# Kernel optimization log

Measured on AMD Instinct MI355X. Metric: run time of the kernel, lower is better.

Reference implementation:

```python
import jax, jax.numpy as jnp
import numpy as np

N = 6144   # number of patches (bag size)
L = 1024   # input feature dim
D = 512    # GCN hidden dim
ALPHA = 0.4
THRESH = 0.5


def _layernorm(x, g, b):
    m = jnp.mean(x, axis=-1, keepdims=True)
    v = jnp.mean((x - m) ** 2, axis=-1, keepdims=True)
    return (x - m) / jnp.sqrt(v + 1e-5) * g + b


def _l1rows(x):
    # F.normalize(x, p=1): row-wise L1 normalize with eps=1e-12
    return x / jnp.maximum(jnp.sum(jnp.abs(x), axis=1, keepdims=True), 1e-12)


def _nonlin(x, w1, b1, g, bn, w2, b2):
    h = jax.nn.relu(_layernorm(x @ w1 + b1, g, bn))
    return h @ w2 + b2


def _gcn(x, adj, w, b, g, bn):
    # GraphConvolution: adj @ (x @ W) + bias, then LayerNorm + ReLU
    return jax.nn.relu(_layernorm(adj @ (x @ w) + b, g, bn))


def setup_inputs() -> dict:
    key = jax.random.key(0)
    ks = iter(jax.random.split(key, 64))

    def nrm(shape, s=0.02):
        return jax.random.normal(next(ks), shape, jnp.float32) * s

    inp = {
        'x_path': jax.random.normal(next(ks), (N, L), jnp.float32),
        'maps': jax.random.uniform(next(ks), (N, N), jnp.float32) * 0.1,
    }
    for pre in ['nl0', 'nl1']:
        inp[pre + '_w1'] = nrm((L, D)); inp[pre + '_b1'] = jnp.zeros((D,), jnp.float32)
        inp[pre + '_g'] = jnp.ones((D,), jnp.float32); inp[pre + '_bn'] = jnp.zeros((D,), jnp.float32)
        inp[pre + '_w2'] = nrm((D, D)); inp[pre + '_b2'] = jnp.zeros((D,), jnp.float32)
    for pre in ['gc0', 'gc1', 'gc2', 'ga0', 'ga1', 'ga2']:
        inp[pre + '_w'] = nrm((D, D)); inp[pre + '_b'] = jnp.zeros((D,), jnp.float32)
        inp[pre + '_g'] = jnp.ones((D,), jnp.float32); inp[pre + '_bn'] = jnp.zeros((D,), jnp.float32)
    inp['attn_wa'] = nrm((L, 256)); inp['attn_ba'] = jnp.zeros((256,), jnp.float32)
    inp['attn_wb'] = nrm((L, 256)); inp['attn_bb'] = jnp.zeros((256,), jnp.float32)
    inp['attn_wc'] = nrm((256, 1)); inp['attn_bc'] = jnp.zeros((1,), jnp.float32)
    inp['cls_w'] = nrm((L, 4), 0.001)
    inp['ln_g'] = jnp.ones((L,), jnp.float32); inp['ln_b'] = jnp.zeros((L,), jnp.float32)
    return inp


def reference(x_path, maps,
              nl0_w1, nl0_b1, nl0_g, nl0_bn, nl0_w2, nl0_b2,
              nl1_w1, nl1_b1, nl1_g, nl1_bn, nl1_w2, nl1_b2,
              gc0_w, gc0_b, gc0_g, gc0_bn,
              gc1_w, gc1_b, gc1_g, gc1_bn,
              gc2_w, gc2_b, gc2_g, gc2_bn,
              ga0_w, ga0_b, ga0_g, ga0_bn,
              ga1_w, ga1_b, ga1_g, ga1_bn,
              ga2_w, ga2_b, ga2_g, ga2_bn,
              attn_wa, attn_ba, attn_wb, attn_bb, attn_wc, attn_bc,
              cls_w, ln_g, ln_b):
    # cosine-similarity adjacency: L2-normalize rows, gram matrix, min-max, threshold
    xn = x_path / jnp.maximum(jnp.linalg.norm(x_path, axis=1, keepdims=True), 1e-12)
    cs = xn @ xn.T                                       # [N,N]
    cs = (cs - cs.min()) / (cs.max() - cs.min())
    cs = (cs >= THRESH).astype(jnp.float32)

    # gated attention (eval mode, no dropout): A = Wc (tanh(Wa x) * sigmoid(Wb x))
    a = jnp.tanh(x_path @ attn_wa + attn_ba)
    bg = jax.nn.sigmoid(x_path @ attn_wb + attn_bb)
    agg = (a * bg) @ attn_wc + attn_bc                   # [N,1]

    s = jax.nn.sigmoid(agg)
    aw = s * s.T                                         # outer product [N,N]
    aw = (aw - aw.min()) / (aw.max() - aw.min())
    aw = ALPHA + (1.0 - ALPHA) * aw + maps

    cs = _l1rows(cs)
    aw = _l1rows(aw)

    x0 = _nonlin(x_path, nl0_w1, nl0_b1, nl0_g, nl0_bn, nl0_w2, nl0_b2)
    x1 = _nonlin(x_path, nl1_w1, nl1_b1, nl1_g, nl1_bn, nl1_w2, nl1_b2)

    g1 = _gcn(x0, cs, gc0_w, gc0_b, gc0_g, gc0_bn)
    g1 = _gcn(g1, cs, gc1_w, gc1_b, gc1_g, gc1_bn)
    g1 = _gcn(g1, cs, gc2_w, gc2_b, gc2_g, gc2_bn)

    g2 = _gcn(x1, aw, ga0_w, ga0_b, ga0_g, ga0_bn)
    g2 = _gcn(g2, aw, ga1_w, ga1_b, ga1_g, ga1_bn)
    g2 = _gcn(g2, aw, ga2_w, ga2_b, ga2_g, ga2_bn)

    gcf = jnp.concatenate([g2, g1], axis=1)              # [N, 1024]

    n = x_path.shape[0]
    trans = (cs @ agg) / (n ** 0.5)                      # [N,1]
    fw = jax.nn.softmax(0.3 * trans + 0.7 * agg, axis=0) # softmax over patches
    pooled = fw.T @ gcf                                  # [1, 1024]
    pooled = _layernorm(pooled, ln_g, ln_b)

    logits = pooled @ cls_w                              # [1, 4]
    y_hat = jnp.argmax(logits, axis=1, keepdims=True)    # topk k=1 index
    hazards = jax.nn.sigmoid(logits)
    surv = jnp.cumprod(1.0 - hazards, axis=1)
    return hazards, surv, y_hat
```

## Files before the change

kernel.cpp:

```cpp
#include <hip/hip_runtime.h>

#define N_ 6144
#define L_ 1024
#define D_ 512
#define H_ 256

typedef unsigned short u16;
typedef __attribute__((ext_vector_type(4))) float f32x4;
typedef __attribute__((ext_vector_type(8))) short s16x8;
typedef __attribute__((ext_vector_type(4))) short s16x4;

__device__ __forceinline__ u16 f2b(float f){
  unsigned u = __float_as_uint(f);
  u += 0x7FFFu + ((u >> 16) & 1u);
  return (u16)(u >> 16);
}
__device__ __forceinline__ float b2f(u16 h){ return __uint_as_float(((unsigned)h) << 16); }
__device__ __forceinline__ unsigned fkey(float f){
  unsigned u = __float_as_uint(f);
  return (u & 0x80000000u) ? ~u : (u | 0x80000000u);
}
__device__ __forceinline__ float funkey(unsigned k){
  unsigned u = (k & 0x80000000u) ? (k & 0x7FFFFFFFu) : ~k;
  return __uint_as_float(u);
}
__device__ __forceinline__ float wave_sum(float v){
  #pragma unroll
  for(int o=32;o;o>>=1) v += __shfl_xor(v,o);
  return v;
}
__device__ __forceinline__ float wave_max(float v){
  #pragma unroll
  for(int o=32;o;o>>=1) v = fmaxf(v,__shfl_xor(v,o));
  return v;
}
__device__ __forceinline__ float wave_min(float v){
  #pragma unroll
  for(int o=32;o;o>>=1) v = fminf(v,__shfl_xor(v,o));
  return v;
}
__device__ __forceinline__ float blk_sum256(float v){
  __shared__ float sm[4];
  v = wave_sum(v);
  __syncthreads();
  if((threadIdx.x&63)==0) sm[threadIdx.x>>6]=v;
  __syncthreads();
  return sm[0]+sm[1]+sm[2]+sm[3];
}
__device__ __forceinline__ float blk_min256(float v){
  __shared__ float sm[4];
  v = wave_min(v);
  __syncthreads();
  if((threadIdx.x&63)==0) sm[threadIdx.x>>6]=v;
  __syncthreads();
  return fminf(fminf(sm[0],sm[1]),fminf(sm[2],sm[3]));
}
__device__ __forceinline__ float blk_max256(float v){
  __shared__ float sm[4];
  v = wave_max(v);
  __syncthreads();
  if((threadIdx.x&63)==0) sm[threadIdx.x>>6]=v;
  __syncthreads();
  return fmaxf(fmaxf(sm[0],sm[1]),fmaxf(sm[2],sm[3]));
}


template<int VW> __device__ __forceinline__ void waitv(){
  if constexpr(VW==8) asm volatile("s_waitcnt vmcnt(8)" ::: "memory");
  else if constexpr(VW==4) asm volatile("s_waitcnt vmcnt(4)" ::: "memory");
  else asm volatile("s_waitcnt vmcnt(0)" ::: "memory");
}

#define STG4(bb,k0) do{ \
  __builtin_amdgcn_global_load_lds((__attribute__((address_space(1))) void*)(gA0+(k0)), (__attribute__((address_space(3))) void*)(lds + (bb)*4096 + (wid<<9)),        16, 0, 0); \
  __builtin_amdgcn_global_load_lds((__attribute__((address_space(1))) void*)(gA1+(k0)), (__attribute__((address_space(3))) void*)(lds + (bb)*4096 + 2048 + (wid<<9)), 16, 0, 0); \
  __builtin_amdgcn_global_load_lds((__attribute__((address_space(1))) void*)(gB0+(k0)), (__attribute__((address_space(3))) void*)(lds + 12288 + (bb)*4096 + (wid<<9)),        16, 0, 0); \
  __builtin_amdgcn_global_load_lds((__attribute__((address_space(1))) void*)(gB1+(k0)), (__attribute__((address_space(3))) void*)(lds + 12288 + (bb)*4096 + 2048 + (wid<<9)), 16, 0, 0); \
}while(0)

template<int MODE>
__global__ __launch_bounds__(256) void gemm_bt(
  const u16* __restrict__ A, const u16* __restrict__ Bt,
  int M, int Nc, int K,
  u16* __restrict__ Cb, unsigned* __restrict__ mmx)
{
  __shared__ __align__(16) u16 lds[3*4096*2];
  const int tid = threadIdx.x;
  const int wid = tid>>6, lane = tid&63;

  const int gx = gridDim.x;
  int lid = blockIdx.y*gx + blockIdx.x;
  const int nwg = gx*gridDim.y;
  if ((nwg & 7) == 0) {
    const int chunk = nwg >> 3;
    lid = (lid & 7)*chunk + (lid >> 3);
  }
  const int m0 = (lid/gx)<<7, n0 = (lid%gx)<<7;
  const int wr = wid>>1, wc = wid&1;

  const int Klen = K / gridDim.z;
  const int kbeg = blockIdx.z * Klen;

  const int srow = (wid<<4) + (lane>>2);
  const int scol = (((lane&3) ^ ((lane>>2)&3))<<3);
  const u16* gA0 = A  + (size_t)(m0+srow   )*K + scol;
  const u16* gA1 = A  + (size_t)(m0+srow+64)*K + scol;
  const u16* gB0 = Bt + (size_t)(n0+srow   )*K + scol;
  const u16* gB1 = Bt + (size_t)(n0+srow+64)*K + scol;

  f32x4 acc[4][4] = {};
  const int lr = lane&15, lk = (lane>>4)<<3;
  const int rdo = lk ^ ((lr&3)<<3);

  const int NIT = Klen>>5;
  STG4(0, kbeg);
  STG4(1, kbeg+32);
  STG4(2, kbeg+64);

  for (int it=0; it<NIT-2; ++it){
    const int b = it - (it/3)*3;
    waitv<8>();
    __builtin_amdgcn_s_barrier();
    const u16* baseA = lds + b*4096;
    const u16* baseB = lds + 12288 + b*4096;
    s16x8 af[4], bfr[4];
    #pragma unroll
    for(int m=0;m<4;m++) af[m]  = *(const s16x8*)(baseA + ((wr<<6)+(m<<4)+lr)*32 + rdo);
    #pragma unroll
    for(int n=0;n<4;n++) bfr[n] = *(const s16x8*)(baseB + ((wc<<6)+(n<<4)+lr)*32 + rdo);
    asm volatile("s_waitcnt lgkmcnt(0)" ::: "memory");
    __builtin_amdgcn_sched_barrier(0);
    __builtin_amdgcn_s_barrier();
    if (it+3 < NIT) STG4(b, kbeg + ((it+3)<<5));
    #pragma unroll
    for(int m=0;m<4;m++)
      #pragma unroll
      for(int n=0;n<4;n++)
        acc[m][n] = __builtin_amdgcn_mfma_f32_16x16x32_bf16(af[m], bfr[n], acc[m][n], 0,0,0);
  }
  {
    const int it = NIT-2; const int b = it - (it/3)*3;
    waitv<4>();
    __builtin_amdgcn_s_barrier();
    const u16* baseA = lds + b*4096;
    const u16* baseB = lds + 12288 + b*4096;
    s16x8 af[4], bfr[4];
    #pragma unroll
    for(int m=0;m<4;m++) af[m]  = *(const s16x8*)(baseA + ((wr<<6)+(m<<4)+lr)*32 + rdo);
    #pragma unroll
    for(int n=0;n<4;n++) bfr[n] = *(const s16x8*)(baseB + ((wc<<6)+(n<<4)+lr)*32 + rdo);
    #pragma unroll
    for(int m=0;m<4;m++)
      #pragma unroll
      for(int n=0;n<4;n++)
        acc[m][n] = __builtin_amdgcn_mfma_f32_16x16x32_bf16(af[m], bfr[n], acc[m][n], 0,0,0);
  }
  {
    const int it = NIT-1; const int b = it - (it/3)*3;
    waitv<0>();
    __builtin_amdgcn_s_barrier();
    const u16* baseA = lds + b*4096;
    const u16* baseB = lds + 12288 + b*4096;
    s16x8 af[4], bfr[4];
    #pragma unroll
    for(int m=0;m<4;m++) af[m]  = *(const s16x8*)(baseA + ((wr<<6)+(m<<4)+lr)*32 + rdo);
    #pragma unroll
    for(int n=0;n<4;n++) bfr[n] = *(const s16x8*)(baseB + ((wc<<6)+(n<<4)+lr)*32 + rdo);
    #pragma unroll
    for(int m=0;m<4;m++)
      #pragma unroll
      for(int n=0;n<4;n++)
        acc[m][n] = __builtin_amdgcn_mfma_f32_16x16x32_bf16(af[m], bfr[n], acc[m][n], 0,0,0);
  }

  float tmin = 3.0e38f, tmax = -3.0e38f;
  if (MODE==1){
    #pragma unroll
    for(int m=0;m<4;m++)
      #pragma unroll
      for(int n=0;n<4;n++){
        f32x4 v = acc[m][n];
        #pragma unroll
        for(int e=0;e<4;e++){ tmin = fminf(tmin,v[e]); tmax = fmaxf(tmax,v[e]); }
      }
  }

  __syncthreads();
  u16* lC = lds;
  {
    const int rb_l = (wr<<6) + ((lane>>4)<<2);
    const int cb_l = (wc<<6) + lr;
    #pragma unroll
    for(int m=0;m<4;m++)
      #pragma unroll
      for(int n=0;n<4;n++){
        f32x4 v = acc[m][n];
        #pragma unroll
        for(int e=0;e<4;e++)
          lC[(rb_l+(m<<4)+e)*128 + cb_l+(n<<4)] = f2b(v[e]);
      }
  }
  __syncthreads();
  u16* Cp = (MODE==0) ? (Cb + (size_t)blockIdx.z * M * Nc) : Cb;
  #pragma unroll
  for(int q=0;q<8;q++){
    int c = (q<<8) + tid;
    int r = c>>4, cc = (c&15)<<3;
    *(s16x8*)(Cp + (size_t)(m0+r)*Nc + n0 + cc) = *(const s16x8*)(lC + r*128 + cc);
  }

  if (MODE==1){
    tmin = wave_min(tmin); tmax = wave_max(tmax);
    __shared__ float rmn[4], rmx[4];
    if(lane==0){ rmn[wid]=tmin; rmx[wid]=tmax; }
    __syncthreads();
    if(tid==0){
      float mn=fminf(fminf(rmn[0],rmn[1]),fminf(rmn[2],rmn[3]));
      float mx=fmaxf(fmaxf(rmx[0],rmx[1]),fmaxf(rmx[2],rmx[3]));
      atomicMin(mmx+0, fkey(mn));
      atomicMax(mmx+1, fkey(mx));
    }
  }
}

__global__ __launch_bounds__(256) void transpose_cast(
  const float* __restrict__ src, u16* __restrict__ dst, int R, int C)
{
  __shared__ float t[32][33];
  int c0 = blockIdx.x<<5, r0 = blockIdx.y<<5;
  int tx = threadIdx.x&31, ty = threadIdx.x>>5;
  #pragma unroll
  for(int i=0;i<32;i+=8) t[ty+i][tx] = src[(size_t)(r0+ty+i)*C + c0+tx];
  __syncthreads();
  #pragma unroll
  for(int i=0;i<32;i+=8) dst[(size_t)(c0+ty+i)*R + r0+tx] = f2b(t[tx][ty+i]);
}

__global__ __launch_bounds__(256) void transpose_sum_bf(
  const u16* __restrict__ src, size_t pstr, int nsp,
  u16* __restrict__ dst, int R, int C)
{
  __shared__ float t[32][33];
  int c0 = blockIdx.x<<5, r0 = blockIdx.y<<5;
  int tx = threadIdx.x&31, ty = threadIdx.x>>5;
  #pragma unroll
  for(int i=0;i<32;i+=8){
    float v = 0;
    for(int p=0;p<nsp;p++)
      v += b2f(src[(size_t)p*pstr + (size_t)(r0+ty+i)*C + c0+tx]);
    t[ty+i][tx] = v;
  }
  __syncthreads();
  #pragma unroll
  for(int i=0;i<32;i+=8) dst[(size_t)(c0+ty+i)*R + r0+tx] = f2b(t[tx][ty+i]);
}

__global__ __launch_bounds__(256) void prep_x(const float* __restrict__ x,
  u16* __restrict__ xb, u16* __restrict__ xnb)
{
  int row = blockIdx.x, t = threadIdx.x;
  const float* p = x + (size_t)row*L_ + (t<<2);
  f32x4 v = *(const f32x4*)p;
  float ss = v[0]*v[0]+v[1]*v[1]+v[2]*v[2]+v[3]*v[3];
  float tot = blk_sum256(ss);
  float inv = 1.0f/fmaxf(sqrtf(tot), 1e-12f);
  u16* pb = xb  + (size_t)row*L_ + (t<<2);
  u16* pn = xnb + (size_t)row*L_ + (t<<2);
  #pragma unroll
  for(int k=0;k<4;k++){ pb[k]=f2b(v[k]); pn[k]=f2b(v[k]*inv); }
}

__global__ __launch_bounds__(256) void attn_epi(const u16* __restrict__ A1, const u16* __restrict__ B1,
  size_t pstr, int nsp,
  const float* __restrict__ ba, const float* __restrict__ bb,
  const float* __restrict__ wc, const float* __restrict__ bc,
  float* __restrict__ agg, float* __restrict__ s)
{
  int row = (blockIdx.x<<2) + (threadIdx.x>>6);
  int lane = threadIdx.x&63;
  float a[4]={0,0,0,0}, b[4]={0,0,0,0};
  for(int p=0;p<nsp;p++){
    s16x4 ua = *(const s16x4*)(A1 + (size_t)p*pstr + (size_t)row*H_ + (lane<<2));
    s16x4 ub = *(const s16x4*)(B1 + (size_t)p*pstr + (size_t)row*H_ + (lane<<2));
    #pragma unroll
    for(int j=0;j<4;j++){ a[j]+=b2f((u16)ua[j]); b[j]+=b2f((u16)ub[j]); }
  }
  float acc=0;
  #pragma unroll
  for(int j=0;j<4;j++){
    int h = (lane<<2)+j;
    float tv = tanhf(a[j]+ba[h]);
    float sg = 1.0f/(1.0f+expf(-(b[j]+bb[h])));
    acc += tv*sg*wc[h];
  }
  acc = wave_sum(acc);
  if(lane==0){
    float v = acc + bc[0];
    agg[row]=v;
    s[row]=1.0f/(1.0f+expf(-v));
  }
}

__global__ __launch_bounds__(256) void s_stats(const float* __restrict__ s, float* __restrict__ sc){
  int t=threadIdx.x;
  float sum=0, mn=3e38f, mx=-3e38f;
  for(int i=t;i<N_;i+=256){ float v=s[i]; sum+=v; mn=fminf(mn,v); mx=fmaxf(mx,v); }
  float S=blk_sum256(sum);
  float MN=blk_min256(mn);
  float MX=blk_max256(mx);
  if(t==0){ sc[0]=S; sc[1]=MN; sc[2]=MX; }
}

__global__ __launch_bounds__(256) void aw_write(const float* __restrict__ maps, const float* __restrict__ s,
  const float* __restrict__ sc, u16* __restrict__ awb)
{
  int i = blockIdx.x, t = threadIdx.x;
  float smin = sc[1], smax = sc[2];
  float mn = smin*smin, mx = smax*smax;
  float beta = 0.6f/(mx-mn);
  float c1 = 0.4f - beta*mn;
  float si = s[i];
  const float* mrow = maps + (size_t)i*N_;
  float mv[24];
  float part = 0;
  #pragma unroll
  for(int q=0;q<24;q++){
    int j = t + (q<<8);
    mv[q] = c1 + beta*si*s[j] + mrow[j];
    part += mv[q];
  }
  float r = blk_sum256(part);
  float inv = 1.0f/fmaxf(r, 1e-12f);
  u16* orow = awb + (size_t)i*N_;
  #pragma unroll
  for(int q=0;q<24;q++) orow[t + (q<<8)] = f2b(mv[q]*inv);
}

__global__ __launch_bounds__(256) void ln_epi512(const u16* __restrict__ Y, size_t pstr, int nsp,
  const float* __restrict__ ki,
  const float* __restrict__ bias, const float* __restrict__ g, const float* __restrict__ bn,
  u16* __restrict__ outb)
{
  int row = (blockIdx.x<<2)+(threadIdx.x>>6);
  int lane = threadIdx.x&63;
  int c0 = lane<<3;
  float v[8] = {0,0,0,0,0,0,0,0};
  for(int p=0;p<nsp;p++){
    s16x8 u = *(const s16x8*)(Y + (size_t)p*pstr + (size_t)row*D_ + c0);
    #pragma unroll
    for(int j=0;j<8;j++) v[j] += b2f((u16)u[j]);
  }
  float scale = ki ? (1.0f/ki[row]) : 1.0f;
  float sum=0, ssum=0;
  #pragma unroll
  for(int j=0;j<8;j++){ v[j] = v[j]*scale + bias[c0+j]; sum+=v[j]; ssum+=v[j]*v[j]; }
  sum = wave_sum(sum); ssum = wave_sum(ssum);
  float m = sum*(1.0f/D_);
  float var = ssum*(1.0f/D_) - m*m;
  float invsd = rsqrtf(var + 1e-5f);
  u16 ob[8];
  #pragma unroll
  for(int j=0;j<8;j++){
    float o = (v[j]-m)*invsd*g[c0+j] + bn[c0+j];
    o = fmaxf(o, 0.0f);
    ob[j] = f2b(o);
  }
  *(s16x8*)(outb + (size_t)row*D_ + c0) = *(s16x8*)ob;
}

__global__ __launch_bounds__(256) void bias_cast(const u16* __restrict__ Y, size_t pstr, int nsp,
  const float* __restrict__ b, u16* __restrict__ outb)
{
  size_t idx = ((size_t)blockIdx.x*256 + threadIdx.x)<<3;
  float v[8] = {0,0,0,0,0,0,0,0};
  for(int p=0;p<nsp;p++){
    s16x8 u = *(const s16x8*)(Y + (size_t)p*pstr + idx);
    #pragma unroll
    for(int j=0;j<8;j++) v[j] += b2f((u16)u[j]);
  }
  int c = (int)(idx & (D_-1));
  u16 ob[8];
  #pragma unroll
  for(int k=0;k<8;k++) ob[k] = f2b(v[k]+b[c+k]);
  *(s16x8*)(outb+idx) = *(s16x8*)ob;
}

__global__ void init_k(unsigned* mmx){ mmx[0]=0xFFFFFFFFu; mmx[1]=0u; }

__global__ __launch_bounds__(256) void binarize(u16* __restrict__ csb,
  const unsigned* __restrict__ mmx, const float* __restrict__ agg,
  float* __restrict__ ki, float* __restrict__ z)
{
  int i = blockIdx.x, t = threadIdx.x;
  float mn = funkey(mmx[0]), mx = funkey(mmx[1]);
  float th = mn + 0.5f*(mx-mn);
  u16* row = csb + (size_t)i*N_;
  float cnt = 0, dot = 0;
  #pragma unroll
  for(int q=0;q<24;q++){
    int j = t + (q<<8);
    bool on = b2f(row[j]) >= th;
    row[j] = on ? (u16)0x3F80 : (u16)0;
    if(on){ cnt += 1.0f; dot += agg[j]; }
  }
  float k = blk_sum256(cnt);
  float dt = blk_sum256(dot);
  if(t==0){
    ki[i] = k;
    float tr = dt/(k*sqrtf((float)N_));
    z[i] = 0.3f*tr + 0.7f*agg[i];
  }
}

__global__ __launch_bounds__(1024) void softmax_prep(const float* __restrict__ z,
  float* __restrict__ e, float* __restrict__ sexp)
{
  int t = threadIdx.x;
  __shared__ float sm[16];
  float mx=-3e38f;
  for(int i=t;i<N_;i+=1024) mx=fmaxf(mx,z[i]);
  mx = wave_max(mx);
  if((t&63)==0) sm[t>>6]=mx;
  __syncthreads();
  float zm = sm[0];
  #pragma unroll
  for(int w=1;w<16;w++) zm=fmaxf(zm,sm[w]);
  __syncthreads();
  float sum=0;
  for(int i=t;i<N_;i+=1024){ float ee=expf(z[i]-zm); e[i]=ee; sum+=ee; }
  sum = wave_sum(sum);
  if((t&63)==0) sm[t>>6]=sum;
  __syncthreads();
  if(t==0){ float S=0; for(int w=0;w<16;w++) S+=sm[w]; *sexp=S; }
}

__global__ __launch_bounds__(256) void pooled_partial(const float* __restrict__ e,
  const u16* __restrict__ g2b, const u16* __restrict__ g1b, float* __restrict__ part)
{
  int b = blockIdx.x, t = threadIdx.x;
  float a0=0,a1=0,a2=0,a3=0;
  for(int r=0;r<24;r++){
    int row = b*24+r;
    float w = e[row];
    a0 += w * b2f(g2b[(size_t)row*D_ + t]);
    a1 += w * b2f(g2b[(size_t)row*D_ + t+256]);
    a2 += w * b2f(g1b[(size_t)row*D_ + t]);
    a3 += w * b2f(g1b[(size_t)row*D_ + t+256]);
  }
  part[(size_t)b*1024 + t]      = a0;
  part[(size_t)b*1024 + t+256]  = a1;
  part[(size_t)b*1024 + t+512]  = a2;
  part[(size_t)b*1024 + t+768]  = a3;
}

__global__ __launch_bounds__(1024) void final_k(const float* __restrict__ part, const float* __restrict__ sexp,
  const float* __restrict__ lng, const float* __restrict__ lnb,
  const float* __restrict__ clsw, float* __restrict__ out)
{
  int t = threadIdx.x;
  __shared__ float red[16];
  __shared__ float smv[1024];
  __shared__ float lgs[4];
  float p=0;
  for(int b=0;b<256;b++) p += part[b*1024 + t];
  p /= sexp[0];
  float w = wave_sum(p);
  if((t&63)==0) red[t>>6]=w;
  __syncthreads();
  float tot=0;
  #pragma unroll
  for(int i2=0;i2<16;i2++) tot+=red[i2];
  float m = tot*(1.0f/1024.0f);
  __syncthreads();
  float d = p-m;
  w = wave_sum(d*d);
  if((t&63)==0) red[t>>6]=w;
  __syncthreads();
  tot=0;
  #pragma unroll
  for(int i2=0;i2<16;i2++) tot+=red[i2];
  float var = tot*(1.0f/1024.0f);
  float y = d*rsqrtf(var+1e-5f)*lng[t] + lnb[t];
  smv[t]=y;
  __syncthreads();
  if(t<4){
    float lg=0;
    for(int j=0;j<1024;j++) lg += smv[j]*clsw[j*4+t];
    lgs[t]=lg;
  }
  __syncthreads();
  if(t==0){
    float h[4];
    int am=0; float best=lgs[0];
    #pragma unroll
    for(int c2=0;c2<4;c2++){ h[c2]=1.0f/(1.0f+expf(-lgs[c2])); if(lgs[c2]>best){best=lgs[c2];am=c2;} }
    float sv=1.0f;
    #pragma unroll
    for(int c2=0;c2<4;c2++){ out[c2]=h[c2]; sv*=(1.0f-h[c2]); out[4+c2]=sv; }
    out[8]=(float)am;
  }
}

extern "C" void kernel_launch(void* const* d_in, const int* in_sizes, int n_in,
                              void* d_out, int out_size, void* d_ws, size_t ws_size,
                              hipStream_t stream)
{
  const float* x_path =(const float*)d_in[0];
  const float* maps   =(const float*)d_in[1];
  const float* nl0_w1 =(const float*)d_in[2];
  const float* nl0_b1 =(const float*)d_in[3];
  const float* nl0_g  =(const float*)d_in[4];
  const float* nl0_bn =(const float*)d_in[5];
  const float* nl0_w2 =(const float*)d_in[6];
  const float* nl0_b2 =(const float*)d_in[7];
  const float* nl1_w1 =(const float*)d_in[8];
  const float* nl1_b1 =(const float*)d_in[9];
  const float* nl1_g  =(const float*)d_in[10];
  const float* nl1_bn =(const float*)d_in[11];
  const float* nl1_w2 =(const float*)d_in[12];
  const float* nl1_b2 =(const float*)d_in[13];
  const float *gw[6], *gb[6], *gg[6], *gbn[6];
  for(int l=0;l<6;l++){
    gw[l]  = (const float*)d_in[14+l*4+0];
    gb[l]  = (const float*)d_in[14+l*4+1];
    gg[l]  = (const float*)d_in[14+l*4+2];
    gbn[l] = (const float*)d_in[14+l*4+3];
  }
  const float* attn_wa=(const float*)d_in[38];
  const float* attn_ba=(const float*)d_in[39];
  const float* attn_wb=(const float*)d_in[40];
  const float* attn_bb=(const float*)d_in[41];
  const float* attn_wc=(const float*)d_in[42];
  const float* attn_bc=(const float*)d_in[43];
  const float* cls_w  =(const float*)d_in[44];
  const float* ln_g   =(const float*)d_in[45];
  const float* ln_b   =(const float*)d_in[46];

  char* ws=(char*)d_ws;
  size_t off=0;
  auto alc=[&](size_t b)->char*{ char* p=ws+off; off=(off+b+255)&~(size_t)255; return p; };
  u16* BIG = (u16*)alc((size_t)N_*N_*2);
  u16* XB  = (u16*)alc((size_t)N_*L_*2);
  u16* XNB = (u16*)alc((size_t)N_*L_*2);
  u16* WT_nl0w1=(u16*)alc((size_t)D_*L_*2);
  u16* WT_nl0w2=(u16*)alc((size_t)D_*D_*2);
  u16* WT_nl1w1=(u16*)alc((size_t)D_*L_*2);
  u16* WT_nl1w2=(u16*)alc((size_t)D_*D_*2);
  u16* WT_g[6];
  for(int l=0;l<6;l++) WT_g[l]=(u16*)alc((size_t)D_*D_*2);
  u16* WT_wa=(u16*)alc((size_t)H_*L_*2);
  u16* WT_wb=(u16*)alc((size_t)H_*L_*2);
  const int SK = 4;
  u16* SP = (u16*)alc((size_t)SK*N_*D_*2);
  u16* XWT=(u16*)alc((size_t)D_*N_*2);
  u16* XA =(u16*)alc((size_t)N_*D_*2);
  u16* XBv=(u16*)alc((size_t)N_*D_*2);
  u16* X0B=(u16*)alc((size_t)N_*D_*2);
  u16* X1B=(u16*)alc((size_t)N_*D_*2);
  float* PART=(float*)alc((size_t)256*1024*4);
  float* AGG=(float*)alc(N_*4);
  float* SS =(float*)alc(N_*4);
  float* KI =(float*)alc(N_*4);
  float* Z  =(float*)alc(N_*4);
  float* E  =(float*)alc(N_*4);
  float* SC =(float*)alc(256);
  unsigned* MMX=(unsigned*)alc(256);
  float* SEXP=(float*)alc(256);

  const size_t PS_D = (size_t)N_*D_;
  const size_t PS_H = (size_t)N_*H_;
  u16* A1 = SP;
  u16* B1 = SP + (size_t)SK*PS_H;

  init_k<<<1,1,0,stream>>>(MMX);
  prep_x<<<N_,256,0,stream>>>(x_path, XB, XNB);

  transpose_cast<<<dim3(D_/32, L_/32),256,0,stream>>>(nl0_w1, WT_nl0w1, L_, D_);
  transpose_cast<<<dim3(D_/32, D_/32),256,0,stream>>>(nl0_w2, WT_nl0w2, D_, D_);
  transpose_cast<<<dim3(D_/32, L_/32),256,0,stream>>>(nl1_w1, WT_nl1w1, L_, D_);
  transpose_cast<<<dim3(D_/32, D_/32),256,0,stream>>>(nl1_w2, WT_nl1w2, D_, D_);
  for(int l=0;l<6;l++)
    transpose_cast<<<dim3(D_/32, D_/32),256,0,stream>>>(gw[l], WT_g[l], D_, D_);
  transpose_cast<<<dim3(H_/32, L_/32),256,0,stream>>>(attn_wa, WT_wa, L_, H_);
  transpose_cast<<<dim3(H_/32, L_/32),256,0,stream>>>(attn_wb, WT_wb, L_, H_);

  gemm_bt<0><<<dim3(H_/128, N_/128, SK),256,0,stream>>>(XB, WT_wa, N_, H_, L_, A1, nullptr);
  gemm_bt<0><<<dim3(H_/128, N_/128, SK),256,0,stream>>>(XB, WT_wb, N_, H_, L_, B1, nullptr);
  attn_epi<<<N_/4,256,0,stream>>>(A1,B1,PS_H,SK,attn_ba,attn_bb,attn_wc,attn_bc,AGG,SS);
  s_stats<<<1,256,0,stream>>>(SS,SC);

  aw_write<<<N_,256,0,stream>>>(maps,SS,SC,BIG);

  gemm_bt<0><<<dim3(D_/128,N_/128,SK),256,0,stream>>>(XB, WT_nl1w1, N_,D_,L_, SP, nullptr);
  ln_epi512<<<N_/4,256,0,stream>>>(SP,PS_D,SK,nullptr,nl1_b1,nl1_g,nl1_bn,XA);
  gemm_bt<0><<<dim3(D_/128,N_/128,SK),256,0,stream>>>(XA, WT_nl1w2, N_,D_,D_, SP, nullptr);
  bias_cast<<<(N_*D_/8)/256,256,0,stream>>>(SP,PS_D,SK, nl1_b2, X1B);

  {
    const u16* cur=X1B;
    for(int l=0;l<3;l++){
      int gi = 3+l;
      gemm_bt<0><<<dim3(D_/128,N_/128,SK),256,0,stream>>>(cur, WT_g[gi], N_,D_,D_, SP, nullptr);
      transpose_sum_bf<<<dim3(D_/32, N_/32),256,0,stream>>>(SP, PS_D, SK, XWT, N_, D_);
      gemm_bt<0><<<dim3(D_/128,N_/128,SK),256,0,stream>>>(BIG, XWT, N_,D_,N_, SP, nullptr);
      u16* nxt = (l==0)? XA : (l==1)? XBv : X1B;
      ln_epi512<<<N_/4,256,0,stream>>>(SP,PS_D,SK, nullptr, gb[gi], gg[gi], gbn[gi], nxt);
      cur = nxt;
    }
  }

  gemm_bt<0><<<dim3(D_/128,N_/128,SK),256,0,stream>>>(XB, WT_nl0w1, N_,D_,L_, SP, nullptr);
  ln_epi512<<<N_/4,256,0,stream>>>(SP,PS_D,SK,nullptr,nl0_b1,nl0_g,nl0_bn,XA);
  gemm_bt<0><<<dim3(D_/128,N_/128,SK),256,0,stream>>>(XA, WT_nl0w2, N_,D_,D_, SP, nullptr);
  bias_cast<<<(N_*D_/8)/256,256,0,stream>>>(SP,PS_D,SK, nl0_b2, X0B);

  gemm_bt<1><<<dim3(N_/128,N_/128,1),256,0,stream>>>(XNB, XNB, N_,N_,L_, BIG, MMX);
  binarize<<<N_,256,0,stream>>>(BIG, MMX, AGG, KI, Z);

  {
    const u16* cur=X0B;
    for(int l=0;l<3;l++){
      int gi = l;
      gemm_bt<0><<<dim3(D_/128,N_/128,SK),256,0,stream>>>(cur, WT_g[gi], N_,D_,D_, SP, nullptr);
      transpose_sum_bf<<<dim3(D_/32, N_/32),256,0,stream>>>(SP, PS_D, SK, XWT, N_, D_);
      gemm_bt<0><<<dim3(D_/128,N_/128,SK),256,0,stream>>>(BIG, XWT, N_,D_,N_, SP, nullptr);
      u16* nxt = (l==0)? XA : (l==1)? XBv : X0B;
      ln_epi512<<<N_/4,256,0,stream>>>(SP,PS_D,SK, KI, gb[gi], gg[gi], gbn[gi], nxt);
      cur = nxt;
    }
  }

  softmax_prep<<<1,1024,0,stream>>>(Z,E,SEXP);
  pooled_partial<<<256,256,0,stream>>>(E,X1B,X0B,PART);
  final_k<<<1,1024,0,stream>>>(PART,SEXP,ln_g,ln_b,cls_w,(float*)d_out);

  (void)in_sizes;(void)n_in;(void)out_size;(void)ws_size;
}
```

Baseline: 914.9 us.

## Fuse input projections into one GEMM and gather sparse rows for binary adjacency

Merges the four x_path projections (attention a/b, nl0_w1, nl1_w1) into a single 1536-wide GEMM with split-K of 2, removing three separate passes over X. Binarize now emits per-row bitmasks and tracks the maximum row degree. When that degree is at most 64, the dense cs adjacency GEMMs and transposes are skipped and replaced by a gather-sum over the set columns. Nontemporal stores are added for the big NxN writes. The sparse path runs only when the runtime degree is small, so the data decides whether it is taken.

After: 869.7 us. 1.05x faster.

```diff
diff --git a/kernel.cpp b/kernel.cpp
--- a/kernel.cpp
+++ b/kernel.cpp
@@ -4,8 +4,10 @@
 #define L_ 1024
 #define D_ 512
 #define H_ 256
+#define SPARSE_MAX 64u
 
 typedef unsigned short u16;
+typedef unsigned long long u64;
 typedef __attribute__((ext_vector_type(4))) float f32x4;
 typedef __attribute__((ext_vector_type(8))) short s16x8;
 typedef __attribute__((ext_vector_type(4))) short s16x4;
@@ -82,8 +84,10 @@
 __global__ __launch_bounds__(256) void gemm_bt(
   const u16* __restrict__ A, const u16* __restrict__ Bt,
   int M, int Nc, int K,
-  u16* __restrict__ Cb, unsigned* __restrict__ mmx)
-{
+  u16* __restrict__ Cb, unsigned* __restrict__ mmx,
+  const unsigned* __restrict__ gate)
+{
+  if (gate && gate[2] <= SPARSE_MAX) return;
   __shared__ __align__(16) u16 lds[3*4096*2];
   const int tid = threadIdx.x;
   const int wid = tid>>6, lane = tid&63;
@@ -206,7 +210,11 @@
   for(int q=0;q<8;q++){
     int c = (q<<8) + tid;
     int r = c>>4, cc = (c&15)<<3;
-    *(s16x8*)(Cp + (size_t)(m0+r)*Nc + n0 + cc) = *(const s16x8*)(lC + r*128 + cc);
+    s16x8 v = *(const s16x8*)(lC + r*128 + cc);
+    if (MODE==1)
+      __builtin_nontemporal_store(v, (s16x8*)(Cp + (size_t)(m0+r)*Nc + n0 + cc));
+    else
+      *(s16x8*)(Cp + (size_t)(m0+r)*Nc + n0 + cc) = v;
   }
 
   if (MODE==1){
@@ -238,8 +246,9 @@
 
 __global__ __launch_bounds__(256) void transpose_sum_bf(
   const u16* __restrict__ src, size_t pstr, int nsp,
-  u16* __restrict__ dst, int R, int C)
-{
+  u16* __restrict__ dst, int R, int C, const unsigned* __restrict__ gate)
+{
+  if (gate && gate[2] <= SPARSE_MAX) return;
   __shared__ float t[32][33];
   int c0 = blockIdx.x<<5, r0 = blockIdx.y<<5;
   int tx = threadIdx.x&31, ty = threadIdx.x>>5;
@@ -270,7 +279,7 @@
   for(int k=0;k<4;k++){ pb[k]=f2b(v[k]); pn[k]=f2b(v[k]*inv); }
 }
 
-__global__ __launch_bounds__(256) void attn_epi(const u16* __restrict__ A1, const u16* __restrict__ B1,
+__global__ __launch_bounds__(256) void attn_epi(const u16* __restrict__ SPA,
   size_t pstr, int nsp,
   const float* __restrict__ ba, const float* __restrict__ bb,
   const float* __restrict__ wc, const float* __restrict__ bc,
@@ -280,8 +289,8 @@
   int lane = threadIdx.x&63;
   float a[4]={0,0,0,0}, b[4]={0,0,0,0};
   for(int p=0;p<nsp;p++){
-    s16x4 ua = *(const s16x4*)(A1 + (size_t)p*pstr + (size_t)row*H_ + (lane<<2));
-    s16x4 ub = *(const s16x4*)(B1 + (size_t)p*pstr + (size_t)row*H_ + (lane<<2));
+    s16x4 ua = *(const s16x4*)(SPA + (size_t)p*pstr + (size_t)row*1536 + (lane<<2));
+    s16x4 ub = *(const s16x4*)(SPA + (size_t)p*pstr + (size_t)row*1536 + 256 + (lane<<2));
     #pragma unroll
     for(int j=0;j<4;j++){ a[j]+=b2f((u16)ua[j]); b[j]+=b2f((u16)ub[j]); }
   }
@@ -333,20 +342,25 @@
   float inv = 1.0f/fmaxf(r, 1e-12f);
   u16* orow = awb + (size_t)i*N_;
   #pragma unroll
-  for(int q=0;q<24;q++) orow[t + (q<<8)] = f2b(mv[q]*inv);
+  for(int q=0;q<24;q++)
+    __builtin_nontemporal_store(f2b(mv[q]*inv), orow + t + (q<<8));
 }
 
 __global__ __launch_bounds__(256) void ln_epi512(const u16* __restrict__ Y, size_t pstr, int nsp,
+  int rs, int cbase,
   const float* __restrict__ ki,
   const float* __restrict__ bias, const float* __restrict__ g, const float* __restrict__ bn,
-  u16* __restrict__ outb)
-{
+  u16* __restrict__ outb,
+  const unsigned* __restrict__ gate, const u16* __restrict__ Yalt)
+{
+  const u16* src = Y; size_t ps = pstr; int np = nsp, rstride = rs, cb = cbase;
+  if (gate && gate[2] <= SPARSE_MAX){ src = Yalt; ps = 0; np = 1; rstride = 512; cb = 0; }
   int row = (blockIdx.x<<2)+(threadIdx.x>>6);
   int lane = threadIdx.x&63;
   int c0 = lane<<3;
   float v[8] = {0,0,0,0,0,0,0,0};
-  for(int p=0;p<nsp;p++){
-    s16x8 u = *(const s16x8*)(Y + (size_t)p*pstr + (size_t)row*D_ + c0);
+  for(int p=0;p<np;p++){
+    s16x8 u = *(const s16x8*)(src + (size_t)p*ps + (size_t)row*rstride + cb + c0);
     #pragma unroll
     for(int j=0;j<8;j++) v[j] += b2f((u16)u[j]);
   }
@@ -385,22 +399,26 @@
   *(s16x8*)(outb+idx) = *(s16x8*)ob;
 }
 
-__global__ void init_k(unsigned* mmx){ mmx[0]=0xFFFFFFFFu; mmx[1]=0u; }
+__global__ void init_k(unsigned* mmx){ mmx[0]=0xFFFFFFFFu; mmx[1]=0u; mmx[2]=0u; }
 
 __global__ __launch_bounds__(256) void binarize(u16* __restrict__ csb,
-  const unsigned* __restrict__ mmx, const float* __restrict__ agg,
-  float* __restrict__ ki, float* __restrict__ z)
+  unsigned* __restrict__ mmx, const float* __restrict__ agg,
+  float* __restrict__ ki, float* __restrict__ z, u64* __restrict__ bm)
 {
   int i = blockIdx.x, t = threadIdx.x;
+  int lane = t&63, w = t>>6;
   float mn = funkey(mmx[0]), mx = funkey(mmx[1]);
   float th = mn + 0.5f*(mx-mn);
   u16* row = csb + (size_t)i*N_;
+  u64* bmrow = bm + (size_t)i*96;
   float cnt = 0, dot = 0;
   #pragma unroll
   for(int q=0;q<24;q++){
     int j = t + (q<<8);
     bool on = b2f(row[j]) >= th;
-    row[j] = on ? (u16)0x3F80 : (u16)0;
+    __builtin_nontemporal_store(on ? (u16)0x3F80 : (u16)0, row + j);
+    u64 mask = __ballot(on);
+    if(lane==0) bmrow[(q<<2)+w] = mask;
     if(on){ cnt += 1.0f; dot += agg[j]; }
   }
   float k = blk_sum256(cnt);
@@ -409,7 +427,45 @@
     ki[i] = k;
     float tr = dt/(k*sqrtf((float)N_));
     z[i] = 0.3f*tr + 0.7f*agg[i];
-  }
+    atomicMax(mmx+2, (unsigned)(k+0.5f));
+  }
+}
+
+__global__ __launch_bounds__(256) void gather_rows(const u64* __restrict__ bm,
+  const u16* __restrict__ SPp, size_t pstr, int nsp,
+  const unsigned* __restrict__ gate, u16* __restrict__ YS)
+{
+  if (gate[2] > SPARSE_MAX) return;
+  int i = blockIdx.x, t = threadIdx.x;
+  __shared__ u64 wbuf[96];
+  __shared__ u16 idx[SPARSE_MAX];
+  __shared__ int nn_s;
+  if (t < 96) wbuf[t] = bm[(size_t)i*96 + t];
+  __syncthreads();
+  if (t == 0){
+    int nn = 0;
+    for(int k=0;k<96;k++){
+      u64 m = wbuf[k];
+      while(m && nn < (int)SPARSE_MAX){
+        int b = __ffsll((long long)m) - 1;
+        m &= m - 1;
+        idx[nn++] = (u16)((k<<6) + b);
+      }
+    }
+    nn_s = nn;
+  }
+  __syncthreads();
+  int nn = nn_s;
+  float a0=0, a1=0;
+  for(int k=0;k<nn;k++){
+    size_t jb = (size_t)idx[k]*512;
+    for(int p=0;p<nsp;p++){
+      a0 += b2f(SPp[p*pstr + jb + t]);
+      a1 += b2f(SPp[p*pstr + jb + t + 256]);
+    }
+  }
+  YS[(size_t)i*512 + t]       = f2b(a0);
+  YS[(size_t)i*512 + t + 256] = f2b(a1);
 }
 
 __global__ __launch_bounds__(1024) void softmax_prep(const float* __restrict__ z,
@@ -542,21 +598,19 @@
   u16* BIG = (u16*)alc((size_t)N_*N_*2);
   u16* XB  = (u16*)alc((size_t)N_*L_*2);
   u16* XNB = (u16*)alc((size_t)N_*L_*2);
-  u16* WT_nl0w1=(u16*)alc((size_t)D_*L_*2);
+  u16* WT_proj=(u16*)alc((size_t)1536*L_*2);
   u16* WT_nl0w2=(u16*)alc((size_t)D_*D_*2);
-  u16* WT_nl1w1=(u16*)alc((size_t)D_*L_*2);
   u16* WT_nl1w2=(u16*)alc((size_t)D_*D_*2);
   u16* WT_g[6];
   for(int l=0;l<6;l++) WT_g[l]=(u16*)alc((size_t)D_*D_*2);
-  u16* WT_wa=(u16*)alc((size_t)H_*L_*2);
-  u16* WT_wb=(u16*)alc((size_t)H_*L_*2);
-  const int SK = 4;
-  u16* SP = (u16*)alc((size_t)SK*N_*D_*2);
+  u16* SP = (u16*)alc((size_t)2*N_*1536*2);
   u16* XWT=(u16*)alc((size_t)D_*N_*2);
-  u16* XA =(u16*)alc((size_t)N_*D_*2);
-  u16* XBv=(u16*)alc((size_t)N_*D_*2);
+  u16* XA0=(u16*)alc((size_t)N_*D_*2);
+  u16* XA1=(u16*)alc((size_t)N_*D_*2);
   u16* X0B=(u16*)alc((size_t)N_*D_*2);
   u16* X1B=(u16*)alc((size_t)N_*D_*2);
+  u16* YS =(u16*)alc((size_t)N_*D_*2);
+  u64* BM =(u64*)alc((size_t)N_*96*8);
   float* PART=(float*)alc((size_t)256*1024*4);
   float* AGG=(float*)alc(N_*4);
   float* SS =(float*)alc(N_*4);
@@ -568,64 +622,60 @@
   float* SEXP=(float*)alc(256);
 
   const size_t PS_D = (size_t)N_*D_;
-  const size_t PS_H = (size_t)N_*H_;
-  u16* A1 = SP;
-  u16* B1 = SP + (size_t)SK*PS_H;
+  const size_t PS_P = (size_t)N_*1536;
 
   init_k<<<1,1,0,stream>>>(MMX);
   prep_x<<<N_,256,0,stream>>>(x_path, XB, XNB);
 
-  transpose_cast<<<dim3(D_/32, L_/32),256,0,stream>>>(nl0_w1, WT_nl0w1, L_, D_);
+  transpose_cast<<<dim3(H_/32, L_/32),256,0,stream>>>(attn_wa, WT_proj,                         L_, H_);
+  transpose_cast<<<dim3(H_/32, L_/32),256,0,stream>>>(attn_wb, WT_proj + (size_t)256*L_,        L_, H_);
+  transpose_cast<<<dim3(D_/32, L_/32),256,0,stream>>>(nl0_w1,  WT_proj + (size_t)512*L_,        L_, D_);
+  transpose_cast<<<dim3(D_/32, L_/32),256,0,stream>>>(nl1_w1,  WT_proj + (size_t)1024*L_,       L_, D_);
   transpose_cast<<<dim3(D_/32, D_/32),256,0,stream>>>(nl0_w2, WT_nl0w2, D_, D_);
-  transpose_cast<<<dim3(D_/32, L_/32),256,0,stream>>>(nl1_w1, WT_nl1w1, L_, D_);
   transpose_cast<<<dim3(D_/32, D_/32),256,0,stream>>>(nl1_w2, WT_nl1w2, D_, D_);
   for(int l=0;l<6;l++)
     transpose_cast<<<dim3(D_/32, D_/32),256,0,stream>>>(gw[l], WT_g[l], D_, D_);
-  transpose_cast<<<dim3(H_/32, L_/32),256,0,stream>>>(attn_wa, WT_wa, L_, H_);
-  transpose_cast<<<dim3(H_/32, L_/32),256,0,stream>>>(attn_wb, WT_wb, L_, H_);
-
-  gemm_bt<0><<<dim3(H_/128, N_/128, SK),256,0,stream>>>(XB, WT_wa, N_, H_, L_, A1, nullptr);
-  gemm_bt<0><<<dim3(H_/128, N_/128, SK),256,0,stream>>>(XB, WT_wb, N_, H_, L_, B1, nullptr);
-  attn_epi<<<N_/4,256,0,stream>>>(A1,B1,PS_H,SK,attn_ba,attn_bb,attn_wc,attn_bc,AGG,SS);
+
+  gemm_bt<0><<<dim3(1536/128, N_/128, 2),256,0,stream>>>(XB, WT_proj, N_, 1536, L_, SP, nullptr, nullptr);
+  attn_epi<<<N_/4,256,0,stream>>>(SP, PS_P, 2, attn_ba, attn_bb, attn_wc, attn_bc, AGG, SS);
   s_stats<<<1,256,0,stream>>>(SS,SC);
-
   aw_write<<<N_,256,0,stream>>>(maps,SS,SC,BIG);
 
-  gemm_bt<0><<<dim3(D_/128,N_/128,SK),256,0,stream>>>(XB, WT_nl1w1, N_,D_,L_, SP, nullptr);
-  ln_epi512<<<N_/4,256,0,stream>>>(SP,PS_D,SK,nullptr,nl1_b1,nl1_g,nl1_bn,XA);
-  gemm_bt<0><<<dim3(D_/128,N_/128,SK),256,0,stream>>>(XA, WT_nl1w2, N_,D_,D_, SP, nullptr);
-  bias_cast<<<(N_*D_/8)/256,256,0,stream>>>(SP,PS_D,SK, nl1_b2, X1B);
+  ln_epi512<<<N_/4,256,0,stream>>>(SP,PS_P,2, 1536,1024, nullptr, nl1_b1,nl1_g,nl1_bn, XA1, nullptr,nullptr);
+  ln_epi512<<<N_/4,256,0,stream>>>(SP,PS_P,2, 1536, 512, nullptr, nl0_b1,nl0_g,nl0_bn, XA0, nullptr,nullptr);
+
+  gemm_bt<0><<<dim3(D_/128,N_/128,4),256,0,stream>>>(XA1, WT_nl1w2, N_,D_,D_, SP, nullptr, nullptr);
+  bias_cast<<<(N_*D_/8)/256,256,0,stream>>>(SP,PS_D,4, nl1_b2, X1B);
 
   {
     const u16* cur=X1B;
     for(int l=0;l<3;l++){
       int gi = 3+l;
-      gemm_bt<0><<<dim3(D_/128,N_/128,SK),256,0,stream>>>(cur, WT_g[gi], N_,D_,D_, SP, nullptr);
-      transpose_sum_bf<<<dim3(D_/32, N_/32),256,0,stream>>>(SP, PS_D, SK, XWT, N_, D_);
-      gemm_bt<0><<<dim3(D_/128,N_/128,SK),256,0,stream>>>(BIG, XWT, N_,D_,N_, SP, nullptr);
-      u16* nxt = (l==0)? XA : (l==1)? XBv : X1B;
-      ln_epi512<<<N_/4,256,0,stream>>>(SP,PS_D,SK, nullptr, gb[gi], gg[gi], gbn[gi], nxt);
+      gemm_bt<0><<<dim3(D_/128,N_/128,4),256,0,stream>>>(cur, WT_g[gi], N_,D_,D_, SP, nullptr, nullptr);
+      transpose_sum_bf<<<dim3(D_/32, N_/32),256,0,stream>>>(SP, PS_D, 4, XWT, N_, D_, nullptr);
+      gemm_bt<0><<<dim3(D_/128,N_/128,4),256,0,stream>>>(BIG, XWT, N_,D_,N_, SP, nullptr, nullptr);
+      u16* nxt = (l==0)? XA1 : (l==1)? YS : X1B;
+      ln_epi512<<<N_/4,256,0,stream>>>(SP,PS_D,4, 512,0, nullptr, gb[gi],gg[gi],gbn[gi], nxt, nullptr,nullptr);
       cur = nxt;
     }
   }
 
-  gemm_bt<0><<<dim3(D_/128,N_/128,SK),256,0,stream>>>(XB, WT_nl0w1, N_,D_,L_, SP, nullptr);
-  ln_epi512<<<N_/4,256,0,stream>>>(SP,PS_D,SK,nullptr,nl0_b1,nl0_g,nl0_bn,XA);
-  gemm_bt<0><<<dim3(D_/128,N_/128,SK),256,0,stream>>>(XA, WT_nl0w2, N_,D_,D_, SP, nullptr);
-  bias_cast<<<(N_*D_/8)/256,256,0,stream>>>(SP,PS_D,SK, nl0_b2, X0B);
-
-  gemm_bt<1><<<dim3(N_/128,N_/128,1),256,0,stream>>>(XNB, XNB, N_,N_,L_, BIG, MMX);
-  binarize<<<N_,256,0,stream>>>(BIG, MMX, AGG, KI, Z);
+  gemm_bt<0><<<dim3(D_/128,N_/128,4),256,0,stream>>>(XA0, WT_nl0w2, N_,D_,D_, SP, nullptr, nullptr);
+  bias_cast<<<(N_*D_/8)/256,256,0,stream>>>(SP,PS_D,4, nl0_b2, X0B);
+
+  gemm_bt<1><<<dim3(N_/128,N_/128,1),256,0,stream>>>(XNB, XNB, N_,N_,L_, BIG, MMX, nullptr);
+  binarize<<<N_,256,0,stream>>>(BIG, MMX, AGG, KI, Z, BM);
 
   {
     const u16* cur=X0B;
     for(int l=0;l<3;l++){
       int gi = l;
-      gemm_bt<0><<<dim3(D_/128,N_/128,SK),256,0,stream>>>(cur, WT_g[gi], N_,D_,D_, SP, nullptr);
-      transpose_sum_bf<<<dim3(D_/32, N_/32),256,0,stream>>>(SP, PS_D, SK, XWT, N_, D_);
-      gemm_bt<0><<<dim3(D_/128,N_/128,SK),256,0,stream>>>(BIG, XWT, N_,D_,N_, SP, nullptr);
-      u16* nxt = (l==0)? XA : (l==1)? XBv : X0B;
-      ln_epi512<<<N_/4,256,0,stream>>>(SP,PS_D,SK, KI, gb[gi], gg[gi], gbn[gi], nxt);
+      gemm_bt<0><<<dim3(D_/128,N_/128,4),256,0,stream>>>(cur, WT_g[gi], N_,D_,D_, SP, nullptr, nullptr);
+      transpose_sum_bf<<<dim3(D_/32, N_/32),256,0,stream>>>(SP, PS_D, 4, XWT, N_, D_, MMX);
+      gemm_bt<0><<<dim3(D_/128,N_/128,4),256,0,stream>>>(BIG, XWT, N_,D_,N_, SP, nullptr, MMX);
+      gather_rows<<<N_,256,0,stream>>>(BM, SP, PS_D, 4, MMX, YS);
+      u16* nxt = (l==0)? XA1 : (l==1)? XA0 : X0B;
+      ln_epi512<<<N_/4,256,0,stream>>>(SP,PS_D,4, 512,0, KI, gb[gi],gg[gi],gbn[gi], nxt, MMX, YS);
       cur = nxt;
     }
   }
```
